# Performance work log

Hardware: AMD Instinct MI355X
Metric: run time of the kernel (lower is better)

## Reference

```python
import jax, jax.numpy as jnp
import numpy as np

# constants from init kwargs
PC_RANGE = np.array([0.0, -40.0, -3.0, 70.4, 40.0, 1.0]).reshape(2, 3)
MAX_DIST = (PC_RANGE[1] - PC_RANGE[0]).astype(np.float32)  # [70.4, 80.0, 4.0]
QUAN_SIZE = 0.4
NHEAD = 8
HPD = 16  # hdim_per_dir = (384 // 8) // 3
TABLE_SIZES = (np.ceil(MAX_DIST * 2 / QUAN_SIZE).astype(np.int64) + 1)  # [353, 401, 21]


def setup_inputs() -> dict:
    key = jax.random.key(0)
    ks = jax.random.split(key, 6)
    N, L = 20000, 32
    relpos = jax.random.normal(ks[0], (N, L, 3), dtype=jnp.float32)
    query_features = jax.random.normal(ks[1], (N, NHEAD, 48), dtype=jnp.float32)
    scaling = jnp.ones((), dtype=jnp.float32)
    query_batch_cnt = jnp.full((4,), N // 4, dtype=jnp.int32)
    table_x = jax.random.normal(ks[2], (int(TABLE_SIZES[0]), NHEAD, HPD), dtype=jnp.float32) * 0.02
    table_y = jax.random.normal(ks[3], (int(TABLE_SIZES[1]), NHEAD, HPD), dtype=jnp.float32) * 0.02
    table_z = jax.random.normal(ks[4], (int(TABLE_SIZES[2]), NHEAD, HPD), dtype=jnp.float32) * 0.02
    return {"relpos": relpos, "query_features": query_features, "scaling": scaling,
            "query_batch_cnt": query_batch_cnt, "table_x": table_x, "table_y": table_y,
            "table_z": table_z}


def reference(relpos, query_features, scaling, query_batch_cnt, table_x, table_y, table_z):
    # normalize + quantize relative positions -> per-axis indices
    max_dist = jnp.asarray(MAX_DIST)
    normed = (relpos + max_dist[None, None, :]) / QUAN_SIZE  # [N, L, 3]
    idx = jnp.floor(normed).astype(jnp.int32)  # [N, L, 3]
    N, nhead, hdim = query_features.shape
    qf = query_features.reshape(N, nhead, 3, HPD)  # split hdim across 3 axes
    out = jnp.zeros(relpos.shape[:2] + (nhead,), dtype=query_features.dtype)
    for a, table in enumerate((table_x, table_y, table_z)):
        ia = jnp.clip(idx[..., a], 0, table.shape[0] - 1)  # [N, L]
        emb = table[ia]  # gather -> [N, L, nhead, HPD]
        out = out + jnp.einsum('nlhd,nhd->nlh', emb, qf[:, :, a, :])
    return out * scaling
```

## Files before the change

### kernel.cpp

```cpp
#include <hip/hip_runtime.h>

#define NH 8
#define LQ 32
#define XW_LO 166
#define YW_LO 190
#define WN 21
#define NROWS 63

typedef float    f32x4 __attribute__((ext_vector_type(4)));
typedef _Float16 f16x4 __attribute__((ext_vector_type(4)));
typedef _Float16 f16x2 __attribute__((ext_vector_type(2)));
typedef _Float16 f16x8 __attribute__((ext_vector_type(8)));

__device__ __forceinline__ f16x4 cvt4(f32x4 g) {
    return (f16x4){(_Float16)g.x, (_Float16)g.y, (_Float16)g.z, (_Float16)g.w};
}

__device__ __forceinline__ f16x8 cvt8(f32x4 a, f32x4 b) {
    return (f16x8){(_Float16)a.x, (_Float16)a.y, (_Float16)a.z, (_Float16)a.w,
                   (_Float16)b.x, (_Float16)b.y, (_Float16)b.z, (_Float16)b.w};
}

__device__ __forceinline__ float dot8h(f16x8 a, f16x8 b) {
    f16x2 a0 = __builtin_shufflevector(a, a, 0, 1);
    f16x2 a1 = __builtin_shufflevector(a, a, 2, 3);
    f16x2 a2 = __builtin_shufflevector(a, a, 4, 5);
    f16x2 a3 = __builtin_shufflevector(a, a, 6, 7);
    f16x2 b0 = __builtin_shufflevector(b, b, 0, 1);
    f16x2 b1 = __builtin_shufflevector(b, b, 2, 3);
    f16x2 b2 = __builtin_shufflevector(b, b, 4, 5);
    f16x2 b3 = __builtin_shufflevector(b, b, 6, 7);
#if __has_builtin(__builtin_amdgcn_fdot2)
    float c = __builtin_amdgcn_fdot2(a3, b3, 0.0f, false);
    c = __builtin_amdgcn_fdot2(a2, b2, c, false);
    c = __builtin_amdgcn_fdot2(a1, b1, c, false);
    c = __builtin_amdgcn_fdot2(a0, b0, c, false);
    return c;
#else
    return (float)a0.x*(float)b0.x + (float)a0.y*(float)b0.y
         + (float)a1.x*(float)b1.x + (float)a1.y*(float)b1.y
         + (float)a2.x*(float)b2.x + (float)a2.y*(float)b2.y
         + (float)a3.x*(float)b3.x + (float)a3.y*(float)b3.y;
#endif
}

__global__ __launch_bounds__(512) void rpe_kernel(
    const float* __restrict__ relpos,
    const float* __restrict__ qfeat,
    const float* __restrict__ scaling,
    const float* __restrict__ tx,
    const float* __restrict__ ty,
    const float* __restrict__ tz,
    float* __restrict__ out, int N)
{
    __shared__ alignas(16) _Float16 W[NROWS * 128];

    const int t = threadIdx.x;

#pragma unroll
    for (int i = 0; i < 4; ++i) {
        int c = t + i * 512;
        if (c < NROWS * 32) {
            int r = c >> 5, p = c & 31;
            const float* src;
            if (r < WN)          src = tx + (size_t)(XW_LO + r) * 128 + p * 4;
            else if (r < 2*WN)   src = ty + (size_t)(YW_LO + (r - WN)) * 128 + p * 4;
            else                 src = tz + (size_t)(r - 2*WN) * 128 + p * 4;
            *(f16x4*)&W[r * 128 + p * 4] = cvt4(*(const f32x4*)src);
        }
    }
    __syncthreads();

    const int lane = t & 63;
    const int w    = t >> 6;
    const int gn   = blockIdx.x * 8 + w;
    const int g    = (lane >> 4) & 3;
    const int k15  = lane & 15;
    const int head = k15 >> 1;
    const int p    = lane & 1;
    const int loff = (g & 1) | ((g & 2) << 3);

    const float* rp = relpos + ((size_t)gn * LQ + (lane & 31)) * 3;
    float rx = rp[0], ry = rp[1], rz = rp[2];
    int ix = min(max((int)floorf((rx + 70.4f) * 2.5f), 0), 352);
    int iy = min(max((int)floorf((ry + 80.0f) * 2.5f), 0), 400);
    int iz = min(max((int)floorf((rz + 4.0f)  * 2.5f), 0), 20);
    unsigned packed = (unsigned)ix | ((unsigned)iy << 9) | ((unsigned)iz << 18);

    const float* qb = qfeat + (size_t)gn * (NH * 48) + head * 48 + p * 8;
    f16x8 qx = cvt8(*(const f32x4*)(qb),      *(const f32x4*)(qb + 4));
    f16x8 qy = cvt8(*(const f32x4*)(qb + 16), *(const f32x4*)(qb + 20));
    f16x8 qz = cvt8(*(const f32x4*)(qb + 32), *(const f32x4*)(qb + 36));

    const float s = scaling[0];
    const char* txb = (const char*)tx + k15 * 32;
    const char* tyb = (const char*)ty + k15 * 32;
    const _Float16* Wl = W + k15 * 8;
    float* outp = out + (size_t)gn * (LQ * NH);

#pragma unroll 4
    for (int i = 0; i < 8; ++i) {
        int l = 2 * i + loff;
        unsigned pk = __shfl((int)packed, l, 64);
        unsigned jx = pk & 511u;
        unsigned jy = (pk >> 9) & 511u;
        unsigned jz = pk >> 18;

        f16x8 ax, ay, az;
        unsigned ox = jx - XW_LO;
        if (ox < WN) ax = *(const f16x8*)(Wl + ox * 128);
        else {
            const char* gp = txb + ((size_t)jx << 9);
            ax = cvt8(*(const f32x4*)gp, *(const f32x4*)(gp + 16));
        }
        unsigned oy = jy - YW_LO;
        if (oy < WN) ay = *(const f16x8*)(Wl + (WN + oy) * 128);
        else {
            const char* gp = tyb + ((size_t)jy << 9);
            ay = cvt8(*(const f32x4*)gp, *(const f32x4*)(gp + 16));
        }
        az = *(const f16x8*)(Wl + (2 * WN + jz) * 128);

        float acc = (dot8h(ax, qx) + dot8h(ay, qy)) + dot8h(az, qz);

        int d = __builtin_amdgcn_update_dpp(0, __float_as_int(acc),
                                            0xB1, 0xF, 0xF, true);
        acc += __int_as_float(d);

        if (p == 0) outp[l * NH + head] = acc * s;
    }
}

extern "C" void kernel_launch(void* const* d_in, const int* in_sizes, int n_in,
                              void* d_out, int out_size, void* d_ws, size_t ws_size,
                              hipStream_t stream) {
    const float* relpos  = (const float*)d_in[0];
    const float* qfeat   = (const float*)d_in[1];
    const float* scaling = (const float*)d_in[2];
    const float* tx      = (const float*)d_in[4];
    const float* ty      = (const float*)d_in[5];
    const float* tz      = (const float*)d_in[6];
    float* out           = (float*)d_out;

    int N = in_sizes[0] / (LQ * 3);
    int blocks = (N + 7) / 8;

    rpe_kernel<<<blocks, 512, 0, stream>>>(relpos, qfeat, scaling, tx, ty, tz, out, N);
}
```

Baseline: 22.63 us.

## Use persistent grid-stride blocks with software-prefetched relpos for the next group

Caps the grid at 1024 blocks and makes each wave loop over query groups with a stride of 8192, so the shared-memory table window is built once per block instead of once per 8 queries. Inside the loop, the relpos values for the next iteration are loaded early so their latency overlaps the current group's gathers and dot products. This amortizes the per-block table conversion and the launch overhead, at the cost of fewer resident waves to hide latency and an uneven tail, since 2500 groups of 8 do not divide evenly across 1024 blocks.

```diff
diff --git a/kernel.cpp b/kernel.cpp
--- a/kernel.cpp
+++ b/kernel.cpp
@@ -6,6 +6,8 @@
 #define YW_LO 190
 #define WN 21
 #define NROWS 63
+#define NBLK 1024
+#define NSTR (NBLK * 8)
 
 typedef float    f32x4 __attribute__((ext_vector_type(4)));
 typedef _Float16 f16x4 __attribute__((ext_vector_type(4)));
@@ -61,73 +63,97 @@
     for (int i = 0; i < 4; ++i) {
         int c = t + i * 512;
         if (c < NROWS * 32) {
-            int r = c >> 5, p = c & 31;
+            int r = c >> 5, pc = c & 31;
             const float* src;
-            if (r < WN)          src = tx + (size_t)(XW_LO + r) * 128 + p * 4;
-            else if (r < 2*WN)   src = ty + (size_t)(YW_LO + (r - WN)) * 128 + p * 4;
-            else                 src = tz + (size_t)(r - 2*WN) * 128 + p * 4;
-            *(f16x4*)&W[r * 128 + p * 4] = cvt4(*(const f32x4*)src);
+            if (r < WN)          src = tx + (size_t)(XW_LO + r) * 128 + pc * 4;
+            else if (r < 2*WN)   src = ty + (size_t)(YW_LO + (r - WN)) * 128 + pc * 4;
+            else                 src = tz + (size_t)(r - 2*WN) * 128 + pc * 4;
+            *(f16x4*)&W[r * 128 + pc * 4] = cvt4(*(const f32x4*)src);
         }
     }
     __syncthreads();
 
     const int lane = t & 63;
-    const int w    = t >> 6;
-    const int gn   = blockIdx.x * 8 + w;
     const int g    = (lane >> 4) & 3;
     const int k15  = lane & 15;
     const int head = k15 >> 1;
     const int p    = lane & 1;
     const int loff = (g & 1) | ((g & 2) << 3);
-
-    const float* rp = relpos + ((size_t)gn * LQ + (lane & 31)) * 3;
-    float rx = rp[0], ry = rp[1], rz = rp[2];
-    int ix = min(max((int)floorf((rx + 70.4f) * 2.5f), 0), 352);
-    int iy = min(max((int)floorf((ry + 80.0f) * 2.5f), 0), 400);
-    int iz = min(max((int)floorf((rz + 4.0f)  * 2.5f), 0), 20);
-    unsigned packed = (unsigned)ix | ((unsigned)iy << 9) | ((unsigned)iz << 18);
-
-    const float* qb = qfeat + (size_t)gn * (NH * 48) + head * 48 + p * 8;
-    f16x8 qx = cvt8(*(const f32x4*)(qb),      *(const f32x4*)(qb + 4));
-    f16x8 qy = cvt8(*(const f32x4*)(qb + 16), *(const f32x4*)(qb + 20));
-    f16x8 qz = cvt8(*(const f32x4*)(qb + 32), *(const f32x4*)(qb + 36));
+    const int lsel = lane & 31;
 
     const float s = scaling[0];
     const char* txb = (const char*)tx + k15 * 32;
     const char* tyb = (const char*)ty + k15 * 32;
     const _Float16* Wl = W + k15 * 8;
-    float* outp = out + (size_t)gn * (LQ * NH);
+
+    int gn = blockIdx.x * 8 + (t >> 6);
+    if (gn >= N) return;
+
+    const float* rp = relpos + ((size_t)gn * LQ + lsel) * 3;
+    float rx = rp[0], ry = rp[1], rz = rp[2];
+
+    while (true) {
+        const float* qb = qfeat + (size_t)gn * (NH * 48) + head * 48 + p * 8;
+        f32x4 q0 = *(const f32x4*)(qb);
+        f32x4 q1 = *(const f32x4*)(qb + 4);
+        f32x4 q2 = *(const f32x4*)(qb + 16);
+        f32x4 q3 = *(const f32x4*)(qb + 20);
+        f32x4 q4 = *(const f32x4*)(qb + 32);
+        f32x4 q5 = *(const f32x4*)(qb + 36);
+
+        int ix = min(max((int)floorf((rx + 70.4f) * 2.5f), 0), 352);
+        int iy = min(max((int)floorf((ry + 80.0f) * 2.5f), 0), 400);
+        int iz = min(max((int)floorf((rz + 4.0f)  * 2.5f), 0), 20);
+        unsigned packed = (unsigned)ix | ((unsigned)iy << 9) | ((unsigned)iz << 18);
+
+        int gn_next = gn + NSTR;
+        bool more = gn_next < N;
+        {
+            int gl = more ? gn_next : gn;
+            const float* rpn = relpos + ((size_t)gl * LQ + lsel) * 3;
+            rx = rpn[0]; ry = rpn[1]; rz = rpn[2];
+        }
+
+        f16x8 qx = cvt8(q0, q1);
+        f16x8 qy = cvt8(q2, q3);
+        f16x8 qz = cvt8(q4, q5);
+
+        float* outp = out + (size_t)gn * (LQ * NH);
 
 #pragma unroll 4
-    for (int i = 0; i < 8; ++i) {
-        int l = 2 * i + loff;
-        unsigned pk = __shfl((int)packed, l, 64);
-        unsigned jx = pk & 511u;
-        unsigned jy = (pk >> 9) & 511u;
-        unsigned jz = pk >> 18;
+        for (int i = 0; i < 8; ++i) {
+            int l = 2 * i + loff;
+            unsigned pk = (unsigned)__shfl((int)packed, l, 64);
+            unsigned jx = pk & 511u;
+            unsigned jy = (pk >> 9) & 511u;
+            unsigned jz = pk >> 18;
 
-        f16x8 ax, ay, az;
-        unsigned ox = jx - XW_LO;
-        if (ox < WN) ax = *(const f16x8*)(Wl + ox * 128);
-        else {
-            const char* gp = txb + ((size_t)jx << 9);
-            ax = cvt8(*(const f32x4*)gp, *(const f32x4*)(gp + 16));
+            f16x8 ax, ay, az;
+            unsigned ox = jx - XW_LO;
+            if (ox < WN) ax = *(const f16x8*)(Wl + ox * 128);
+            else {
+                const char* gp = txb + ((size_t)jx << 9);
+                ax = cvt8(*(const f32x4*)gp, *(const f32x4*)(gp + 16));
+            }
+            unsigned oy = jy - YW_LO;
+            if (oy < WN) ay = *(const f16x8*)(Wl + (WN + oy) * 128);
+            else {
+                const char* gp = tyb + ((size_t)jy << 9);
+                ay = cvt8(*(const f32x4*)gp, *(const f32x4*)(gp + 16));
+            }
+            az = *(const f16x8*)(Wl + (2 * WN + jz) * 128);
+
+            float acc = (dot8h(ax, qx) + dot8h(ay, qy)) + dot8h(az, qz);
+
+            int d = __builtin_amdgcn_update_dpp(0, __float_as_int(acc),
+                                                0xB1, 0xF, 0xF, true);
+            acc += __int_as_float(d);
+
+            if (p == 0) outp[l * NH + head] = acc * s;
         }
-        unsigned oy = jy - YW_LO;
-        if (oy < WN) ay = *(const f16x8*)(Wl + (WN + oy) * 128);
-        else {
-            const char* gp = tyb + ((size_t)jy << 9);
-            ay = cvt8(*(const f32x4*)gp, *(const f32x4*)(gp + 16));
-        }
-        az = *(const f16x8*)(Wl + (2 * WN + jz) * 128);
 
-        float acc = (dot8h(ax, qx) + dot8h(ay, qy)) + dot8h(az, qz);
-
-        int d = __builtin_amdgcn_update_dpp(0, __float_as_int(acc),
-                                            0xB1, 0xF, 0xF, true);
-        acc += __int_as_float(d);
-
-        if (p == 0) outp[l * NH + head] = acc * s;
+        if (!more) break;
+        gn = gn_next;
     }
 }
 
@@ -144,6 +170,7 @@
 
     int N = in_sizes[0] / (LQ * 3);
     int blocks = (N + 7) / 8;
+    if (blocks > NBLK) blocks = NBLK;
 
     rpe_kernel<<<blocks, 512, 0, stream>>>(relpos, qfeat, scaling, tx, ty, tz, out, N);
 }
```

After: 21.50 us. 1.05x faster.
